# Kernel optimization log

Measured on AMD Instinct MI355X. Metric: run time of the kernel, lower is better.

The kernel has to match this reference:

```python
import jax, jax.numpy as jnp
import numpy as np

EPS = 1e-05


def setup_inputs() -> dict:
    key = jax.random.key(0)
    B, T, C = 8, 8192, 512
    x = jax.random.normal(key, (B, T, C), dtype=jnp.float32)
    # Learned per-channel scale; module initializes it to ones.
    weight = jnp.ones((C,), dtype=jnp.float32)
    return {"x": x, "weight": weight}


def reference(x, weight):
    """Cumulative (running) group norm over the frame axis.

    x: [B, T, C]; stats are accumulated over channels AND all frames <= t.
    """
    input_dtype = x.dtype
    xc = x.astype(jnp.float32)
    B, T, C = xc.shape

    # Per-frame channel sum, then cumulative sum over time -> [B, T, 1]
    cum_sum = jnp.cumsum(jnp.sum(xc, axis=-1, keepdims=True), axis=1)
    # Element count up to frame t: (t+1) * C (mask is all-ones here)
    cum_count = (jnp.arange(1, T + 1, dtype=jnp.float32) * C).reshape(1, T, 1)
    cum_count = jnp.maximum(cum_count, 1.0)

    cum_mean = cum_sum / cum_count  # [B, T, 1]

    # Squared deviation from the *running* mean, summed over channels, cumsum over time.
    sq_diff = jnp.square(xc - cum_mean)  # [B, T, C]
    cum_var = jnp.cumsum(jnp.sum(sq_diff, axis=-1, keepdims=True), axis=1) / cum_count

    normalized = (xc - cum_mean) * jax.lax.rsqrt(cum_var + EPS)
    out = normalized * weight.astype(jnp.float32)  # broadcast over [B, T, C]
    return out.astype(input_dtype)
```

## Files before the change

### kernel.cpp

```cpp
#include <hip/hip_runtime.h>

#define EPS 1e-5f

typedef float nfloat4 __attribute__((ext_vector_type(4)));


__global__ __launch_bounds__(256) void frame_stats_kernel(
    const float* __restrict__ x, float* __restrict__ s_arr,
    float* __restrict__ q_arr) {
  const int wave = threadIdx.x >> 6;
  const int lane = threadIdx.x & 63;
  const int frame = blockIdx.x * 4 + wave;
  const nfloat4* xb = (const nfloat4*)(x + (size_t)frame * 512);
  nfloat4 a = xb[lane];
  nfloat4 b = xb[64 + lane];
  float s = a.x + a.y + a.z + a.w + b.x + b.y + b.z + b.w;
  float q = a.x * a.x + a.y * a.y + a.z * a.z + a.w * a.w +
            b.x * b.x + b.y * b.y + b.z * b.z + b.w * b.w;
#pragma unroll
  for (int off = 32; off >= 1; off >>= 1) {
    s += __shfl_down(s, off);
    q += __shfl_down(q, off);
  }
  if (lane == 0) {
    s_arr[frame] = s;
    q_arr[frame] = q;
  }
}

__global__ __launch_bounds__(1024) void scan_kernel(
    const float* __restrict__ s_arr, const float* __restrict__ q_arr,
    float* __restrict__ mean_arr, float* __restrict__ inv_arr) {
  const int T = 8192;
  const int b = blockIdx.x;
  const int tid = threadIdx.x;
  const int lane = tid & 63;
  const int wid = tid >> 6;

  __shared__ float lds_s[16];
  __shared__ float lds_v[16];

  const nfloat4* s4p = (const nfloat4*)(s_arr + (size_t)b * T);
  const nfloat4* q4p = (const nfloat4*)(q_arr + (size_t)b * T);
  nfloat4* m4p = (nfloat4*)(mean_arr + (size_t)b * T);
  nfloat4* i4p = (nfloat4*)(inv_arr + (size_t)b * T);

  nfloat4 sa = s4p[2 * tid];
  nfloat4 sb = s4p[2 * tid + 1];
  nfloat4 qa = q4p[2 * tid];
  nfloat4 qb = q4p[2 * tid + 1];

  float p0 = sa.x;
  float p1 = p0 + sa.y;
  float p2 = p1 + sa.z;
  float p3 = p2 + sa.w;
  float p4 = p3 + sb.x;
  float p5 = p4 + sb.y;
  float p6 = p5 + sb.z;
  float p7 = p6 + sb.w;
  float tot = p7, incl = tot;
#pragma unroll
  for (int off = 1; off < 64; off <<= 1) {
    float n = __shfl_up(incl, off);
    if (lane >= off) incl += n;
  }
  if (lane == 63) lds_s[wid] = incl;
  __syncthreads();
  float waveExcl = 0.f;
#pragma unroll
  for (int wv = 0; wv < 16; ++wv)
    if (wv < wid) waveExcl += lds_s[wv];
  float base = waveExcl + incl - tot;

  const int t0 = tid << 3;
  float c0 = (float)(t0 + 1) * 512.f;
  float c1 = (float)(t0 + 2) * 512.f;
  float c2 = (float)(t0 + 3) * 512.f;
  float c3 = (float)(t0 + 4) * 512.f;
  float c4 = (float)(t0 + 5) * 512.f;
  float c5 = (float)(t0 + 6) * 512.f;
  float c6 = (float)(t0 + 7) * 512.f;
  float c7 = (float)(t0 + 8) * 512.f;
  float m0 = (base + p0) / c0;
  float m1 = (base + p1) / c1;
  float m2 = (base + p2) / c2;
  float m3 = (base + p3) / c3;
  float m4 = (base + p4) / c4;
  float m5 = (base + p5) / c5;
  float m6 = (base + p6) / c6;
  float m7 = (base + p7) / c7;

  float v0 = qa.x - 2.f * m0 * sa.x + 512.f * m0 * m0;
  float v1 = qa.y - 2.f * m1 * sa.y + 512.f * m1 * m1;
  float v2 = qa.z - 2.f * m2 * sa.z + 512.f * m2 * m2;
  float v3 = qa.w - 2.f * m3 * sa.w + 512.f * m3 * m3;
  float v4 = qb.x - 2.f * m4 * sb.x + 512.f * m4 * m4;
  float v5 = qb.y - 2.f * m5 * sb.y + 512.f * m5 * m5;
  float v6 = qb.z - 2.f * m6 * sb.z + 512.f * m6 * m6;
  float v7 = qb.w - 2.f * m7 * sb.w + 512.f * m7 * m7;

  float r0 = v0;
  float r1 = r0 + v1;
  float r2 = r1 + v2;
  float r3 = r2 + v3;
  float r4 = r3 + v4;
  float r5 = r4 + v5;
  float r6 = r5 + v6;
  float r7 = r6 + v7;
  float totv = r7, inclv = totv;
#pragma unroll
  for (int off = 1; off < 64; off <<= 1) {
    float n = __shfl_up(inclv, off);
    if (lane >= off) inclv += n;
  }
  if (lane == 63) lds_v[wid] = inclv;
  __syncthreads();
  float waveExclV = 0.f;
#pragma unroll
  for (int wv = 0; wv < 16; ++wv)
    if (wv < wid) waveExclV += lds_v[wv];
  float baseV = waveExclV + inclv - totv;

  nfloat4 moa, mob, ioa, iob;
  moa.x = m0; moa.y = m1; moa.z = m2; moa.w = m3;
  mob.x = m4; mob.y = m5; mob.z = m6; mob.w = m7;
  ioa.x = rsqrtf((baseV + r0) / c0 + EPS);
  ioa.y = rsqrtf((baseV + r1) / c1 + EPS);
  ioa.z = rsqrtf((baseV + r2) / c2 + EPS);
  ioa.w = rsqrtf((baseV + r3) / c3 + EPS);
  iob.x = rsqrtf((baseV + r4) / c4 + EPS);
  iob.y = rsqrtf((baseV + r5) / c5 + EPS);
  iob.z = rsqrtf((baseV + r6) / c6 + EPS);
  iob.w = rsqrtf((baseV + r7) / c7 + EPS);
  m4p[2 * tid] = moa;
  m4p[2 * tid + 1] = mob;
  i4p[2 * tid] = ioa;
  i4p[2 * tid + 1] = iob;
}

__global__ __launch_bounds__(256) void apply_kernel(
    const float* __restrict__ x, const float* __restrict__ weight,
    const float* __restrict__ mean_arr, const float* __restrict__ inv_arr,
    float* __restrict__ out) {
  const long i = (long)blockIdx.x * blockDim.x + threadIdx.x;
  const int frame = (int)(i >> 7);
  const int c4 = (int)(i & 127);
  nfloat4 xv = ((const nfloat4*)x)[i];
  nfloat4 wv = ((const nfloat4*)weight)[c4];
  float m = mean_arr[frame];
  float inv = inv_arr[frame];
  nfloat4 o;
  o.x = (xv.x - m) * inv * wv.x;
  o.y = (xv.y - m) * inv * wv.y;
  o.z = (xv.z - m) * inv * wv.z;
  o.w = (xv.w - m) * inv * wv.w;
  __builtin_nontemporal_store(o, (nfloat4*)out + i);
}

extern "C" void kernel_launch(void* const* d_in, const int* in_sizes, int n_in,
                              void* d_out, int out_size, void* d_ws,
                              size_t ws_size, hipStream_t stream) {
  const float* x = (const float*)d_in[0];
  const float* w = (const float*)d_in[1];
  float* out = (float*)d_out;
  const int B = 8, T = 8192;
  const int BT = B * T;

  float* s_arr = (float*)d_ws;
  float* q_arr = s_arr + BT;
  float* mean_arr = q_arr + BT;
  float* inv_arr = mean_arr + BT;

  frame_stats_kernel<<<BT / 4, 256, 0, stream>>>(x, s_arr, q_arr);
  scan_kernel<<<B, 1024, 0, stream>>>(s_arr, q_arr, mean_arr, inv_arr);
  const long n4 = (long)BT * 128;
  apply_kernel<<<(int)(n4 / 256), 256, 0, stream>>>(x, w, mean_arr, inv_arr,
                                                    out);
}
```

Baseline: 248.1 us.

## Fuse scan and apply kernels with redundant per-block scans over slices

The separate scan and apply kernels are merged. 512 blocks each redo the full per-batch prefix scan of the frame sums, keep the mean and inverse std for their own 128-frame slice in LDS, and then normalize that slice. This drops one kernel launch, the round trip of the mean and inverse arrays through memory, and the single-wave-per-batch scan kernel, which used only 8 blocks. In exchange each block repeats the full 8192-element scan, 64 times per batch, and the apply phase runs with far fewer blocks of 1024 threads.

```diff
diff --git a/kernel.cpp b/kernel.cpp
--- a/kernel.cpp
+++ b/kernel.cpp
@@ -28,22 +28,24 @@
   }
 }
 
-__global__ __launch_bounds__(1024) void scan_kernel(
+__global__ __launch_bounds__(1024) void scan_apply_kernel(
+    const float* __restrict__ x, const float* __restrict__ w,
     const float* __restrict__ s_arr, const float* __restrict__ q_arr,
-    float* __restrict__ mean_arr, float* __restrict__ inv_arr) {
+    float* __restrict__ out) {
   const int T = 8192;
-  const int b = blockIdx.x;
   const int tid = threadIdx.x;
   const int lane = tid & 63;
   const int wid = tid >> 6;
+  const int b = blockIdx.x >> 6;
+  const int slice = blockIdx.x & 63;
 
   __shared__ float lds_s[16];
   __shared__ float lds_v[16];
+  __shared__ float lds_m[128];
+  __shared__ float lds_i[128];
 
   const nfloat4* s4p = (const nfloat4*)(s_arr + (size_t)b * T);
   const nfloat4* q4p = (const nfloat4*)(q_arr + (size_t)b * T);
-  nfloat4* m4p = (nfloat4*)(mean_arr + (size_t)b * T);
-  nfloat4* i4p = (nfloat4*)(inv_arr + (size_t)b * T);
 
   nfloat4 sa = s4p[2 * tid];
   nfloat4 sb = s4p[2 * tid + 1];
@@ -121,40 +123,47 @@
     if (wv < wid) waveExclV += lds_v[wv];
   float baseV = waveExclV + inclv - totv;
 
-  nfloat4 moa, mob, ioa, iob;
-  moa.x = m0; moa.y = m1; moa.z = m2; moa.w = m3;
-  mob.x = m4; mob.y = m5; mob.z = m6; mob.w = m7;
-  ioa.x = rsqrtf((baseV + r0) / c0 + EPS);
-  ioa.y = rsqrtf((baseV + r1) / c1 + EPS);
-  ioa.z = rsqrtf((baseV + r2) / c2 + EPS);
-  ioa.w = rsqrtf((baseV + r3) / c3 + EPS);
-  iob.x = rsqrtf((baseV + r4) / c4 + EPS);
-  iob.y = rsqrtf((baseV + r5) / c5 + EPS);
-  iob.z = rsqrtf((baseV + r6) / c6 + EPS);
-  iob.w = rsqrtf((baseV + r7) / c7 + EPS);
-  m4p[2 * tid] = moa;
-  m4p[2 * tid + 1] = mob;
-  i4p[2 * tid] = ioa;
-  i4p[2 * tid + 1] = iob;
-}
+  const int sliceFirstThread = slice << 4;
+  if ((tid >> 4) == slice) {
+    const int k = (tid - sliceFirstThread) << 3;
+    lds_m[k + 0] = m0;
+    lds_m[k + 1] = m1;
+    lds_m[k + 2] = m2;
+    lds_m[k + 3] = m3;
+    lds_m[k + 4] = m4;
+    lds_m[k + 5] = m5;
+    lds_m[k + 6] = m6;
+    lds_m[k + 7] = m7;
+    lds_i[k + 0] = rsqrtf((baseV + r0) / c0 + EPS);
+    lds_i[k + 1] = rsqrtf((baseV + r1) / c1 + EPS);
+    lds_i[k + 2] = rsqrtf((baseV + r2) / c2 + EPS);
+    lds_i[k + 3] = rsqrtf((baseV + r3) / c3 + EPS);
+    lds_i[k + 4] = rsqrtf((baseV + r4) / c4 + EPS);
+    lds_i[k + 5] = rsqrtf((baseV + r5) / c5 + EPS);
+    lds_i[k + 6] = rsqrtf((baseV + r6) / c6 + EPS);
+    lds_i[k + 7] = rsqrtf((baseV + r7) / c7 + EPS);
+  }
+  __syncthreads();
 
-__global__ __launch_bounds__(256) void apply_kernel(
-    const float* __restrict__ x, const float* __restrict__ weight,
-    const float* __restrict__ mean_arr, const float* __restrict__ inv_arr,
-    float* __restrict__ out) {
-  const long i = (long)blockIdx.x * blockDim.x + threadIdx.x;
-  const int frame = (int)(i >> 7);
-  const int c4 = (int)(i & 127);
-  nfloat4 xv = ((const nfloat4*)x)[i];
-  nfloat4 wv = ((const nfloat4*)weight)[c4];
-  float m = mean_arr[frame];
-  float inv = inv_arr[frame];
-  nfloat4 o;
-  o.x = (xv.x - m) * inv * wv.x;
-  o.y = (xv.y - m) * inv * wv.y;
-  o.z = (xv.z - m) * inv * wv.z;
-  o.w = (xv.w - m) * inv * wv.w;
-  __builtin_nontemporal_store(o, (nfloat4*)out + i);
+  const size_t base4 = ((size_t)b * 8192 + (size_t)slice * 128) * 128;
+  const nfloat4 wv4 = ((const nfloat4*)w)[tid & 127];
+  const nfloat4* x4 = (const nfloat4*)x;
+  nfloat4* out4 = (nfloat4*)out;
+#pragma unroll 4
+  for (int k = 0; k < 16; ++k) {
+    const size_t idx = base4 + (size_t)(k << 10) + tid;
+    const int frame_local = (int)((idx >> 7) & 127) ;
+    nfloat4 xv = x4[idx];
+    const float m = lds_m[(k << 3) + (tid >> 7)];
+    const float iv = lds_i[(k << 3) + (tid >> 7)];
+    (void)frame_local;
+    nfloat4 o;
+    o.x = (xv.x - m) * iv * wv4.x;
+    o.y = (xv.y - m) * iv * wv4.y;
+    o.z = (xv.z - m) * iv * wv4.z;
+    o.w = (xv.w - m) * iv * wv4.w;
+    __builtin_nontemporal_store(o, out4 + idx);
+  }
 }
 
 extern "C" void kernel_launch(void* const* d_in, const int* in_sizes, int n_in,
@@ -163,17 +172,11 @@
   const float* x = (const float*)d_in[0];
   const float* w = (const float*)d_in[1];
   float* out = (float*)d_out;
-  const int B = 8, T = 8192;
-  const int BT = B * T;
+  const int BT = 65536;
 
   float* s_arr = (float*)d_ws;
   float* q_arr = s_arr + BT;
-  float* mean_arr = q_arr + BT;
-  float* inv_arr = mean_arr + BT;
 
   frame_stats_kernel<<<BT / 4, 256, 0, stream>>>(x, s_arr, q_arr);
-  scan_kernel<<<B, 1024, 0, stream>>>(s_arr, q_arr, mean_arr, inv_arr);
-  const long n4 = (long)BT * 128;
-  apply_kernel<<<(int)(n4 / 256), 256, 0, stream>>>(x, w, mean_arr, inv_arr,
-                                                    out);
+  scan_apply_kernel<<<512, 1024, 0, stream>>>(x, w, s_arr, q_arr, out);
 }
```

Result: no change. 247.9 us (-0.1%).
